# Kernel tuning notes

Measured on AMD Instinct MI355X. Metric: run time of the kernel, lower is better.

## Reference

```python
import jax, jax.numpy as jnp
import numpy as np

NEG_INF = -100000000.0
N, L, E, DIM, V_IN, V_OUT = 64, 512, 128, 512, 32000, 10000
D = 2 * DIM  # encoder output feature dim


def _lstm_layer(x, Wih, Whh, bih, bhh, reverse=False):
    """Single-direction LSTM over (N, L, I) -> (N, L, H). PyTorch gate order i,f,g,o."""
    n = x.shape[0]
    H = Whh.shape[1]
    xg = jnp.einsum('nli,gi->nlg', x, Wih) + bih  # precompute input projections (N, L, 4H)

    def step(carry, g_in):
        h, c = carry
        g = g_in + h @ Whh.T + bhh
        i, f, gg, o = jnp.split(g, 4, axis=-1)
        c = jax.nn.sigmoid(f) * c + jax.nn.sigmoid(i) * jnp.tanh(gg)
        h = jax.nn.sigmoid(o) * jnp.tanh(c)
        return (h, c), h

    init = (jnp.zeros((n, H), x.dtype), jnp.zeros((n, H), x.dtype))
    _, hs = jax.lax.scan(step, init, jnp.swapaxes(xg, 0, 1), reverse=reverse)
    return jnp.swapaxes(hs, 0, 1)


def setup_inputs() -> dict:
    key = jax.random.key(0)
    ks = iter(jax.random.split(key, 40))

    def p(shape):
        return (jax.random.normal(next(ks), shape, jnp.float32) * 0.05)

    inp = {}
    inp['X'] = jax.random.randint(next(ks), (N, L), 0, V_IN)
    sl = jax.random.randint(next(ks), (N,), 1, L + 1)
    inp['seq_len'] = sl.at[0].set(L)  # ensure max length == L as the torch code assumes
    inp['embed_W'] = p((V_IN, E))
    # encoder layer 0 (input E, hidden DIM), fwd + bwd directions
    for tag, I in (('l0f', E), ('l0b', E), ('l1f', D), ('l1b', D)):
        inp[tag + '_Wih'] = p((4 * DIM, I))
        inp[tag + '_Whh'] = p((4 * DIM, DIM))
        inp[tag + '_bih'] = p((4 * DIM,))
        inp[tag + '_bhh'] = p((4 * DIM,))
    for tag in ('Ws', 'Wa', 'Ua'):
        inp[tag + '_W'] = p((D, D))
        inp[tag + '_b'] = p((D,))
    inp['va_W'] = p((1, D))
    inp['va_b'] = p((1,))
    inp['dec_Wih'] = p((4 * D, D))
    inp['dec_Whh'] = p((4 * D, D))
    inp['dec_bih'] = p((4 * D,))
    inp['dec_bhh'] = p((4 * D,))
    inp['cls_W'] = p((V_OUT, D))
    inp['cls_b'] = p((V_OUT,))
    return inp


def reference(X, seq_len, embed_W,
              l0f_Wih, l0f_Whh, l0f_bih, l0f_bhh,
              l0b_Wih, l0b_Whh, l0b_bih, l0b_bhh,
              l1f_Wih, l1f_Whh, l1f_bih, l1f_bhh,
              l1b_Wih, l1b_Whh, l1b_bih, l1b_bhh,
              Ws_W, Ws_b, Wa_W, Wa_b, Ua_W, Ua_b, va_W, va_b,
              dec_Wih, dec_Whh, dec_bih, dec_bhh, cls_W, cls_b):
    emb = embed_W[X]  # (N, L, E)
    h0 = jnp.concatenate([
        _lstm_layer(emb, l0f_Wih, l0f_Whh, l0f_bih, l0f_bhh, reverse=False),
        _lstm_layer(emb, l0b_Wih, l0b_Whh, l0b_bih, l0b_bhh, reverse=True)], axis=-1)
    hid = jnp.concatenate([
        _lstm_layer(h0, l1f_Wih, l1f_Whh, l1f_bih, l1f_bhh, reverse=False),
        _lstm_layer(h0, l1b_Wih, l1b_Whh, l1b_bih, l1b_bhh, reverse=True)], axis=-1)  # (N, L, 2*dim)

    ll = hid.shape[1]
    mask = (jnp.arange(ll)[None, :] >= seq_len[:, None]).astype(hid.dtype)  # 1 where padded
    Ua_h = hid @ Ua_W.T + Ua_b  # hoisted: U_a(hid) is loop-invariant
    s_i = jnp.tanh(hid[:, 0] @ Ws_W.T + Ws_b)  # (N, D)

    outs = []
    for _ in range(11):
        e = (jnp.tanh((s_i @ Wa_W.T + Wa_b)[:, None, :] + Ua_h) @ va_W.T + va_b)[..., 0]  # (N, L)
        att = jax.nn.softmax(e + NEG_INF * mask, axis=-1)
        ci = jnp.einsum('nl,nld->nd', att, hid)  # context (N, D)
        # single-step decoder LSTM; cell state reset to zero each step (as in torch code)
        g = ci @ dec_Wih.T + dec_bih + s_i @ dec_Whh.T + dec_bhh
        i, f, gg, o = jnp.split(g, 4, axis=-1)
        c = jax.nn.sigmoid(i) * jnp.tanh(gg)  # f * 0 == 0
        s_i = jax.nn.sigmoid(o) * jnp.tanh(c)
        outs.append(s_i)

    s = jnp.stack(outs, axis=1)  # (N, 11, D)
    return s @ cls_W.T + cls_b  # (N, 11, num_outclass)
```

## Files before the change

kernel.cpp:

```cpp
#include <hip/hip_runtime.h>
#include <stdint.h>

#define NEG_INF -100000000.0f

typedef unsigned short u16;
typedef unsigned long long u64;
typedef __attribute__((ext_vector_type(8))) short v8s;
typedef __attribute__((ext_vector_type(4))) short v4s;
typedef __attribute__((ext_vector_type(4))) float v4f;

__device__ __forceinline__ float bf2f(u16 h){ return __uint_as_float(((unsigned)h)<<16); }
__device__ __forceinline__ u16 f2bf(float f){
  unsigned u = __float_as_uint(f);
  u = u + 0x7fffu + ((u>>16)&1u);
  return (u16)(u>>16);
}
__device__ __forceinline__ float sigm(float x){ return 1.0f/(1.0f+__expf(-x)); }
__device__ __forceinline__ float ftanh(float x){
  x = fminf(15.0f, fmaxf(-15.0f, x));
  float e = __expf(2.0f*x);
  return (e-1.0f)/(e+1.0f);
}

__device__ __forceinline__ void store_h16(u16* p, u64 a, u64 b){
  __hip_atomic_store((u64*)p,     a, __ATOMIC_RELAXED, __HIP_MEMORY_SCOPE_AGENT);
  __hip_atomic_store((u64*)(p+4), b, __ATOMIC_RELAXED, __HIP_MEMORY_SCOPE_AGENT);
}

struct CvtTab {
  const float* src[31];
  unsigned off[31];
  unsigned n[31];
  unsigned total;
};

__global__ __launch_bounds__(256) void cvt_all(CvtTab tab, u16* __restrict__ arena){
  unsigned e0 = (blockIdx.x*256u + threadIdx.x)*8u;
  if (e0 >= tab.total) return;
  int s = 0;
#pragma unroll 1
  for (int i = 1; i < 31; ++i) if (e0 >= tab.off[i]) s = i;
  unsigned rel = e0 - tab.off[s];
  const float* sp = tab.src[s] + rel;
  unsigned nn = tab.n[s];
  union { u16 h[8]; v8s v; } o;
  if (rel + 8 <= nn) {
    float4 a = *(const float4*)sp;
    float4 b = *(const float4*)(sp+4);
    o.h[0]=f2bf(a.x); o.h[1]=f2bf(a.y); o.h[2]=f2bf(a.z); o.h[3]=f2bf(a.w);
    o.h[4]=f2bf(b.x); o.h[5]=f2bf(b.y); o.h[6]=f2bf(b.z); o.h[7]=f2bf(b.w);
  } else {
#pragma unroll
    for (int k = 0; k < 8; ++k) o.h[k] = (rel + k < nn) ? f2bf(sp[k]) : (u16)0;
  }
  *(v8s*)(arena + e0) = o.v;
}

#define GF_OUTBF16 1
#define GF_TANH    2
#define GF_ACCUM   4

__global__ __launch_bounds__(256) void gemm_bf16(
    const u16* __restrict__ A, long long lda,
    const u16* __restrict__ B,
    const u16* __restrict__ bias1, const u16* __restrict__ bias2,
    void* __restrict__ Cout, long long ldc,
    int M, int Nn, int K, int flags)
{
  __shared__ u16 As[8192];
  __shared__ u16 Bs[8192];
  int tid = threadIdx.x;
  int lane = tid & 63, w = tid >> 6;
  int wm = w >> 1, wn = w & 1;
  int bm = blockIdx.x * 128, bn = blockIdx.y * 128;

  v4f acc[4][4];
#pragma unroll
  for (int i=0;i<4;++i)
#pragma unroll
    for (int j=0;j<4;++j) acc[i][j] = (v4f){0.f,0.f,0.f,0.f};

#pragma unroll 1
  for (int ko = 0; ko < K; ko += 64) {
    __syncthreads();
#pragma unroll
    for (int it = 0; it < 8; ++it) {
      int c = tid + 256*it;
      int half = c >> 10;
      int cc = c & 1023;
      int r = cc >> 3;
      int kcb = cc & 7;
      const u16* src;
      if (half == 0) {
        int row = min(bm + r, M-1);
        src = A + (size_t)row*(size_t)lda + ko + (kcb<<3);
      } else {
        int row = min(bn + r, Nn-1);
        src = B + (size_t)row*(size_t)K + ko + (kcb<<3);
      }
      v8s v = *(const v8s*)src;
      char* base = (char*)(half ? Bs : As);
      *(v8s*)(base + (r<<7) + ((kcb<<4) ^ ((r&7)<<4))) = v;
    }
    __syncthreads();
#pragma unroll
    for (int ks = 0; ks < 2; ++ks) {
      v8s af[4], bfr[4];
#pragma unroll
      for (int mt=0; mt<4; ++mt) {
        int r = wm*64 + mt*16 + (lane & 15);
        int kb = (ks<<6) + ((lane>>4)<<4);
        af[mt] = *(const v8s*)((const char*)As + (r<<7) + (kb ^ ((r&7)<<4)));
      }
#pragma unroll
      for (int nt=0; nt<4; ++nt) {
        int r = wn*64 + nt*16 + (lane & 15);
        int kb = (ks<<6) + ((lane>>4)<<4);
        bfr[nt] = *(const v8s*)((const char*)Bs + (r<<7) + (kb ^ ((r&7)<<4)));
      }
#pragma unroll
      for (int mt=0; mt<4; ++mt)
#pragma unroll
        for (int nt=0; nt<4; ++nt)
          acc[mt][nt] = __builtin_amdgcn_mfma_f32_16x16x32_bf16(af[mt], bfr[nt], acc[mt][nt], 0,0,0);
    }
  }

#pragma unroll
  for (int mt=0; mt<4; ++mt) {
#pragma unroll
    for (int nt=0; nt<4; ++nt) {
      int col = bn + wn*64 + nt*16 + (lane&15);
      if (col >= Nn) continue;
      float b = 0.f;
      if (bias1) b += bf2f(bias1[col]);
      if (bias2) b += bf2f(bias2[col]);
#pragma unroll
      for (int r=0; r<4; ++r) {
        int row = bm + wm*64 + mt*16 + ((lane>>4)<<2) + r;
        if (row >= M) continue;
        float v = acc[mt][nt][r] + b;
        if (flags & GF_ACCUM) v += ((float*)Cout)[(size_t)row*(size_t)ldc + col];
        if (flags & GF_TANH) v = ftanh(v);
        if (flags & GF_OUTBF16) ((u16*)Cout)[(size_t)row*(size_t)ldc + col] = f2bf(v);
        else                    ((float*)Cout)[(size_t)row*(size_t)ldc + col] = v;
      }
    }
  }
}

template<int LAYER>
__global__ __launch_bounds__(256, 1) void lstm_scan(
    const u16* __restrict__ xsrc,
    const int* __restrict__ Xidx,
    const u16* __restrict__ Wih_f, const u16* __restrict__ Wih_b,
    const u16* __restrict__ Whh_f, const u16* __restrict__ Whh_b,
    const u16* __restrict__ bih_f, const u16* __restrict__ bhh_f,
    const u16* __restrict__ bih_b, const u16* __restrict__ bhh_b,
    u16* __restrict__ hbuf,
    unsigned* __restrict__ prog)
{
  constexpr int KX  = (LAYER==0) ? 128 : 1024;
  constexpr int NKC = KX/64;
  __shared__ float glds[8*32*18];
  __shared__ u16   hlds[1024];

  const int tid = threadIdx.x, lane = tid & 63, w = tid >> 6;
  const int kh = w >> 1, gp = w & 1;
  const int dir = blockIdx.x >> 6, bg = (blockIdx.x >> 5) & 1, ug = blockIdx.x & 31;
  const int an = lane & 15, hi = lane >> 4, ak = hi << 3;
  const u16* Wih = dir ? Wih_b : Wih_f;
  const u16* Whh = dir ? Whh_b : Whh_f;
  const int gid = dir*2 + bg;
  unsigned* gprog = prog + gid*32;

  const int g = 2*gp + (an>>3);

  v8s wih_reg[2][NKC];
#pragma unroll
  for (int nt = 0; nt < 2; ++nt) {
    const u16* wp = Wih + ((size_t)g*512 + ug*16 + nt*8 + (an&7))*KX + kh*(KX/2);
#pragma unroll
    for (int kc = 0; kc < NKC; ++kc) {
      wih_reg[nt][kc] = *(const v8s*)(wp + kc*32 + ak);
      asm volatile("" : "+v"(wih_reg[nt][kc]));
    }
  }
  v8s whh_reg[2][8];
#pragma unroll
  for (int nt = 0; nt < 2; ++nt) {
    const u16* wp = Whh + ((size_t)g*512 + ug*16 + nt*8 + (an&7))*512 + kh*256;
#pragma unroll
    for (int kc = 0; kc < 8; ++kc) {
      whh_reg[nt][kc] = *(const v8s*)(wp + kc*32 + ak);
      asm volatile("" : "+v"(whh_reg[nt][kc]));
    }
  }

  const int u_pw = tid & 15, n2 = tid >> 4;
  const int uj_pw = ug*16 + u_pw;
  float bsum[4];
  {
    const u16* bi = dir ? bih_b : bih_f;
    const u16* bh = dir ? bhh_b : bhh_f;
#pragma unroll
    for (int q = 0; q < 4; ++q)
      bsum[q] = bf2f(bi[q*512 + uj_pw]) + bf2f(bh[q*512 + uj_pw]);
  }
  float creg[2] = {0.f, 0.f};

  v8s xreg[2][NKC];
  {
    const int t0 = dir ? 511 : 0;
#pragma unroll
    for (int mt = 0; mt < 2; ++mt) {
      int ng = bg*32 + mt*16 + an;
      const u16* xr;
      if constexpr (LAYER == 0) xr = xsrc + (size_t)Xidx[ng*512 + t0]*128 + kh*64;
      else                      xr = xsrc + ((size_t)(ng*512 + t0) << 10) + kh*512;
#pragma unroll
      for (int kc = 0; kc < NKC; ++kc) xreg[mt][kc] = *(const v8s*)(xr + kc*32 + ak);
    }
  }

  for (int step = 0; step < 512; ++step) {
    const int t     = dir ? (511 - step) : step;
    const int tprev = dir ? (t + 1) : (t - 1);

    v4f acc[2][2];
#pragma unroll
    for (int i=0;i<2;++i){ acc[i][0]=(v4f){0,0,0,0}; acc[i][1]=(v4f){0,0,0,0}; }

    if (step > 0) {
      {
        const u64* pl = (const u64*)gprog;
        int spins = 0;
        for (;;) {
          u64 v = ~0ull;
          if (lane < 16)
            v = __hip_atomic_load(pl + lane, __ATOMIC_RELAXED, __HIP_MEMORY_SCOPE_AGENT);
          bool ok = ((unsigned)v >= (unsigned)step) && ((unsigned)(v>>32) >= (unsigned)step);
          if (__all(ok)) break;
          if (++spins > 4) __builtin_amdgcn_s_sleep(1);
        }
        asm volatile("" ::: "memory");
      }

      v8s haf[2][8];
#pragma unroll
      for (int mt = 0; mt < 2; ++mt) {
        int ng = bg*32 + mt*16 + an;
        const u16* hr = hbuf + ((size_t)(ng*512 + tprev) << 10) + dir*512 + kh*256;
#pragma unroll
        for (int kc = 0; kc < 8; ++kc) haf[mt][kc] = *(const v8s*)(hr + kc*32 + ak);
      }
#pragma unroll
      for (int kc = 0; kc < NKC; ++kc)
#pragma unroll
        for (int nt = 0; nt < 2; ++nt)
#pragma unroll
          for (int mt = 0; mt < 2; ++mt)
            acc[mt][nt] = __builtin_amdgcn_mfma_f32_16x16x32_bf16(xreg[mt][kc], wih_reg[nt][kc], acc[mt][nt], 0,0,0);
#pragma unroll
      for (int kc = 0; kc < 8; ++kc)
#pragma unroll
        for (int nt = 0; nt < 2; ++nt)
#pragma unroll
          for (int mt = 0; mt < 2; ++mt)
            acc[mt][nt] = __builtin_amdgcn_mfma_f32_16x16x32_bf16(haf[mt][kc], whh_reg[nt][kc], acc[mt][nt], 0,0,0);
    } else {
#pragma unroll
      for (int kc = 0; kc < NKC; ++kc)
#pragma unroll
        for (int nt = 0; nt < 2; ++nt)
#pragma unroll
          for (int mt = 0; mt < 2; ++mt)
            acc[mt][nt] = __builtin_amdgcn_mfma_f32_16x16x32_bf16(xreg[mt][kc], wih_reg[nt][kc], acc[mt][nt], 0,0,0);
    }

#pragma unroll
    for (int mt=0; mt<2; ++mt)
#pragma unroll
      for (int nt=0; nt<2; ++nt)
#pragma unroll
        for (int r=0; r<4; ++r) {
          int n = mt*16 + hi*4 + r;
          int u = nt*8 + (an&7);
          glds[((kh*4 + g)*32 + n)*18 + u] = acc[mt][nt][r];
        }
    __syncthreads();

#pragma unroll
    for (int k = 0; k < 2; ++k) {
      int n = k*16 + n2;
      float g0 = glds[(0*32+n)*18+u_pw] + glds[(4*32+n)*18+u_pw] + bsum[0];
      float g1 = glds[(1*32+n)*18+u_pw] + glds[(5*32+n)*18+u_pw] + bsum[1];
      float g2 = glds[(2*32+n)*18+u_pw] + glds[(6*32+n)*18+u_pw] + bsum[2];
      float g3 = glds[(3*32+n)*18+u_pw] + glds[(7*32+n)*18+u_pw] + bsum[3];
      float cn = sigm(g1)*creg[k] + sigm(g0)*ftanh(g2);
      creg[k] = cn;
      hlds[n*16 + u_pw] = f2bf(sigm(g3)*ftanh(cn));
    }

    if (lane < 16) {
      int j = lane >> 1;
      int n = 4*w + (j & 3) + 16*(j >> 2);
      int half = lane & 1;
      u64 a = *(const u64*)&hlds[n*16 + half*8];
      u64 b = *(const u64*)&hlds[n*16 + half*8 + 4];
      store_h16(hbuf + ((size_t)((bg*32+n)*512 + t) << 10) + dir*512 + ug*16 + half*8, a, b);
    }

    if (step < 511) {
      const int tn = dir ? (t - 1) : (t + 1);
#pragma unroll
      for (int mt = 0; mt < 2; ++mt) {
        int ng = bg*32 + mt*16 + an;
        const u16* xr;
        if constexpr (LAYER == 0) xr = xsrc + (size_t)Xidx[ng*512 + tn]*128 + kh*64;
        else                      xr = xsrc + ((size_t)(ng*512 + tn) << 10) + kh*512;
#pragma unroll
        for (int kc = 0; kc < NKC; ++kc) xreg[mt][kc] = *(const v8s*)(xr + kc*32 + ak);
      }
    }

    asm volatile("s_waitcnt vmcnt(0)" ::: "memory");
    __syncthreads();

    if (tid == 0)
      __hip_atomic_store(gprog + ug, (unsigned)(step+1), __ATOMIC_RELAXED, __HIP_MEMORY_SCOPE_AGENT);
  }
}

__global__ __launch_bounds__(256) void attn_step(
    const float* __restrict__ qbuf, const u16* __restrict__ Uah,
    const u16* __restrict__ hid, const int* __restrict__ seq_len,
    const u16* __restrict__ vaW, const u16* __restrict__ vab,
    u16* __restrict__ catb)
{
  int n = blockIdx.x, tid = threadIdx.x;
  __shared__ float qs[1024];
  __shared__ float vas[1024];
  __shared__ float es[512];
  __shared__ float red[8];
  for (int d=tid; d<1024; d+=256){ qs[d]=qbuf[n*1024+d]; vas[d]=bf2f(vaW[d]); }
  __syncthreads();
  int sl = seq_len[n];
  float vb = bf2f(vab[0]);
  for (int l=tid; l<512; l+=256) {
    const u16* up = Uah + ((size_t)n*512 + l)*1024;
    float a = 0.f;
    for (int d=0; d<1024; d+=8) {
      v8s uv = *(const v8s*)(up + d);
#pragma unroll
      for (int e=0;e<8;++e)
        a = fmaf(ftanh(bf2f((u16)uv[e]) + qs[d+e]), vas[d+e], a);
    }
    float ev = a + vb;
    if (l >= sl) ev += NEG_INF;
    es[l] = ev;
  }
  __syncthreads();
  float m = -3.4e38f;
  for (int l=tid; l<512; l+=256) m = fmaxf(m, es[l]);
#pragma unroll
  for (int off=1; off<64; off<<=1) m = fmaxf(m, __shfl_xor(m, off));
  if ((tid&63)==0) red[tid>>6] = m;
  __syncthreads();
  m = fmaxf(fmaxf(red[0],red[1]), fmaxf(red[2],red[3]));
  float s = 0.f;
  for (int l=tid; l<512; l+=256){ float p = __expf(es[l]-m); es[l]=p; s+=p; }
#pragma unroll
  for (int off=1; off<64; off<<=1) s += __shfl_xor(s, off);
  if ((tid&63)==0) red[4+(tid>>6)] = s;
  __syncthreads();
  float inv = 1.f/(red[4]+red[5]+red[6]+red[7]);
  int d0 = tid*4;
  float c0=0,c1=0,c2=0,c3=0;
  for (int l=0; l<512; ++l) {
    float a = es[l];
    const u16* hp = hid + ((size_t)n*512 + l)*1024 + d0;
    v4s hv = *(const v4s*)hp;
    c0 = fmaf(a, bf2f((u16)hv[0]), c0);
    c1 = fmaf(a, bf2f((u16)hv[1]), c1);
    c2 = fmaf(a, bf2f((u16)hv[2]), c2);
    c3 = fmaf(a, bf2f((u16)hv[3]), c3);
  }
  catb[n*2048 + d0 + 0] = f2bf(c0*inv);
  catb[n*2048 + d0 + 1] = f2bf(c1*inv);
  catb[n*2048 + d0 + 2] = f2bf(c2*inv);
  catb[n*2048 + d0 + 3] = f2bf(c3*inv);
}

__global__ void dec_pw(const float* __restrict__ g, u16* __restrict__ scat,
                       u16* __restrict__ catb, int it)
{
  int idx = blockIdx.x*256 + threadIdx.x;
  int n = idx >> 10, d = idx & 1023;
  float gi = g[(size_t)n*4096 + d];
  float gg = g[(size_t)n*4096 + 2048 + d];
  float go = g[(size_t)n*4096 + 3072 + d];
  float c = sigm(gi)*ftanh(gg);
  float s = sigm(go)*ftanh(c);
  u16 hb = f2bf(s);
  scat[((size_t)n*11 + it)*1024 + d] = hb;
  catb[n*2048 + 1024 + d] = hb;
}

__global__ void fill_sentinel(float* out, int nel){
  int i = blockIdx.x*256 + threadIdx.x;
  if (i < nel) out[i] = 12345.0f;
}

extern "C" void kernel_launch(void* const* d_in, const int* in_sizes, int n_in,
                              void* d_out, int out_size, void* d_ws, size_t ws_size,
                              hipStream_t stream)
{
  const int* X      = (const int*)d_in[0];
  const int* seqlen = (const int*)d_in[1];
  float* out = (float*)d_out;
  char* ws = (char*)d_ws;

  struct Seg { int idx; int n; };
  static const Seg segs[31] = {
    {2, 4096000},
    {3, 262144},{4,1048576},{5,2048},{6,2048},
    {7, 262144},{8,1048576},{9,2048},{10,2048},
    {11,2097152},{12,1048576},{13,2048},{14,2048},
    {15,2097152},{16,1048576},{17,2048},{18,2048},
    {19,1048576},{20,1024},
    {21,1048576},{22,1024},
    {23,1048576},{24,1024},
    {25,1024},{26,1},
    {27,4194304},{28,4194304},{29,4096},{30,4096},
    {31,10240000},{32,10000},
  };
  const u16* bp[33];
  CvtTab tab;
  size_t aoff = 0;
  for (int i = 0; i < 31; ++i) {
    bp[segs[i].idx] = (const u16*)(ws) + aoff;
    tab.src[i] = (const float*)d_in[segs[i].idx];
    tab.off[i] = (unsigned)aoff;
    tab.n[i]   = (unsigned)segs[i].n;
    aoff += (size_t)((segs[i].n + 7) & ~7);
  }
  tab.total = (unsigned)aoff;
  size_t arena_bytes = ((aoff*2 + 255) & ~(size_t)255);

  const size_t H0_OFF   = arena_bytes;
  const size_t HID_OFF  = H0_OFF   + 67108864;
  const size_t BAR_OFF  = HID_OFF  + 67108864;
  const size_t CATB_OFF = BAR_OFF  + 16384;
  const size_t QBUF_OFF = CATB_OFF + 262144;
  const size_t GDEC_OFF = QBUF_OFF + 262144;
  const size_t SCAT_OFF = GDEC_OFF + 1048576;
  const size_t NEED     = SCAT_OFF + 1441792;

  if (ws_size < NEED) {
    fill_sentinel<<<(out_size+255)/256, 256, 0, stream>>>(out, out_size);
    return;
  }

  u16*      h0   = (u16*)(ws + H0_OFF);
  u16*      Uah  = (u16*)(ws + H0_OFF);
  u16*      hid  = (u16*)(ws + HID_OFF);
  unsigned* bar  = (unsigned*)(ws + BAR_OFF);
  u16*      catb = (u16*)(ws + CATB_OFF);
  float*    qbuf = (float*)(ws + QBUF_OFF);
  float*    gdec = (float*)(ws + GDEC_OFF);
  u16*      scat = (u16*)(ws + SCAT_OFF);

  hipMemsetAsync(ws + BAR_OFF, 0, 16384, stream);

  {
    unsigned nth = (unsigned)(aoff / 8);
    cvt_all<<<(nth + 255)/256, 256, 0, stream>>>(tab, (u16*)ws);
  }

  lstm_scan<0><<<128, 256, 0, stream>>>(
      bp[2], X, bp[3], bp[7], bp[4], bp[8],
      bp[5], bp[6], bp[9], bp[10], h0, bar);

  lstm_scan<1><<<128, 256, 0, stream>>>(
      h0, nullptr, bp[11], bp[15], bp[12], bp[16],
      bp[13], bp[14], bp[17], bp[18], hid, bar + 1024);

  gemm_bf16<<<dim3(256,8), 256, 0, stream>>>(hid, 1024, bp[23], bp[24], nullptr,
      Uah, 1024, 32768, 1024, 1024, GF_OUTBF16);
  gemm_bf16<<<dim3(1,8), 256, 0, stream>>>(hid, 524288, bp[19], bp[20], nullptr,
      catb + 1024, 2048, 64, 1024, 1024, GF_OUTBF16 | GF_TANH);

  for (int it = 0; it < 11; ++it) {
    gemm_bf16<<<dim3(1,8), 256, 0, stream>>>(catb + 1024, 2048, bp[21], bp[22], nullptr,
        qbuf, 1024, 64, 1024, 1024, 0);
    attn_step<<<64, 256, 0, stream>>>(qbuf, Uah, hid, seqlen, bp[25], bp[26], catb);
    gemm_bf16<<<dim3(1,32), 256, 0, stream>>>(catb, 2048, bp[27], bp[29], bp[30],
        gdec, 4096, 64, 4096, 1024, 0);
    gemm_bf16<<<dim3(1,32), 256, 0, stream>>>(catb + 1024, 2048, bp[28], nullptr, nullptr,
        gdec, 4096, 64, 4096, 1024, GF_ACCUM);
    dec_pw<<<256, 256, 0, stream>>>(gdec, scat, catb, it);
  }

  gemm_bf16<<<dim3(6,79), 256, 0, stream>>>(scat, 1024, bp[31], bp[32], nullptr,
      out, 10000, 704, 10000, 1024, 0);
}
```

Measured before the change: 9.742 ms.

## Split LSTM scan work by hidden units instead of batch groups per block

Each block now owns 8 hidden units for all 64 batch rows (two 32-row chunks processed in sequence) instead of 16 units for 32 rows, so each direction spans 64 unit blocks and the batch split is gone. This halves the weight registers per block. Each block now waits on and updates both progress groups, and layer 1 loads its input activations inline each step instead of prefetching them one step ahead. The change trades register pressure for more serial work per step and more cross-block synchronisation traffic.

```diff
diff --git a/kernel.cpp b/kernel.cpp
--- a/kernel.cpp
+++ b/kernel.cpp
@@ -162,43 +162,43 @@
 {
   constexpr int KX  = (LAYER==0) ? 128 : 1024;
   constexpr int NKC = KX/64;
-  __shared__ float glds[8*32*18];
-  __shared__ u16   hlds[1024];
+  __shared__ float glds[2][8*32*10];
+  __shared__ u16   hlds[2][256];
 
   const int tid = threadIdx.x, lane = tid & 63, w = tid >> 6;
   const int kh = w >> 1, gp = w & 1;
-  const int dir = blockIdx.x >> 6, bg = (blockIdx.x >> 5) & 1, ug = blockIdx.x & 31;
+  const int dir = blockIdx.x >> 6, ug = blockIdx.x & 63;
   const int an = lane & 15, hi = lane >> 4, ak = hi << 3;
   const u16* Wih = dir ? Wih_b : Wih_f;
   const u16* Whh = dir ? Whh_b : Whh_f;
-  const int gid = dir*2 + bg;
-  unsigned* gprog = prog + gid*32;
+  const int gidA = dir*2, gidB = dir*2 + 1;
+  unsigned* progA = prog + gidA*64;
+  unsigned* progB = prog + gidB*64;
 
   const int g = 2*gp + (an>>3);
-
-  v8s wih_reg[2][NKC];
-#pragma unroll
-  for (int nt = 0; nt < 2; ++nt) {
-    const u16* wp = Wih + ((size_t)g*512 + ug*16 + nt*8 + (an&7))*KX + kh*(KX/2);
+  const size_t jrow = (size_t)g*512 + ug*8 + (an&7);
+
+  v8s wih_reg[NKC];
+  {
+    const u16* wp = Wih + jrow*KX + kh*(KX/2);
 #pragma unroll
     for (int kc = 0; kc < NKC; ++kc) {
-      wih_reg[nt][kc] = *(const v8s*)(wp + kc*32 + ak);
-      asm volatile("" : "+v"(wih_reg[nt][kc]));
-    }
-  }
-  v8s whh_reg[2][8];
-#pragma unroll
-  for (int nt = 0; nt < 2; ++nt) {
-    const u16* wp = Whh + ((size_t)g*512 + ug*16 + nt*8 + (an&7))*512 + kh*256;
+      wih_reg[kc] = *(const v8s*)(wp + kc*32 + ak);
+      asm volatile("" : "+v"(wih_reg[kc]));
+    }
+  }
+  v8s whh_reg[8];
+  {
+    const u16* wp = Whh + jrow*512 + kh*256;
 #pragma unroll
     for (int kc = 0; kc < 8; ++kc) {
-      whh_reg[nt][kc] = *(const v8s*)(wp + kc*32 + ak);
-      asm volatile("" : "+v"(whh_reg[nt][kc]));
-    }
-  }
-
-  const int u_pw = tid & 15, n2 = tid >> 4;
-  const int uj_pw = ug*16 + u_pw;
+      whh_reg[kc] = *(const v8s*)(wp + kc*32 + ak);
+      asm volatile("" : "+v"(whh_reg[kc]));
+    }
+  }
+
+  const int u_pw = tid & 7, n2 = tid >> 3;
+  const int uj_pw = ug*8 + u_pw;
   float bsum[4];
   {
     const u16* bi = dir ? bih_b : bih_f;
@@ -209,118 +209,140 @@
   }
   float creg[2] = {0.f, 0.f};
 
-  v8s xreg[2][NKC];
-  {
+  constexpr int XC = (LAYER==0) ? 2 : 1;
+  v8s xreg[2][2][XC];
+  if constexpr (LAYER == 0) {
     const int t0 = dir ? 511 : 0;
 #pragma unroll
-    for (int mt = 0; mt < 2; ++mt) {
-      int ng = bg*32 + mt*16 + an;
-      const u16* xr;
-      if constexpr (LAYER == 0) xr = xsrc + (size_t)Xidx[ng*512 + t0]*128 + kh*64;
-      else                      xr = xsrc + ((size_t)(ng*512 + t0) << 10) + kh*512;
-#pragma unroll
-      for (int kc = 0; kc < NKC; ++kc) xreg[mt][kc] = *(const v8s*)(xr + kc*32 + ak);
-    }
+    for (int c = 0; c < 2; ++c)
+#pragma unroll
+      for (int mt = 0; mt < 2; ++mt) {
+        int ng = c*32 + mt*16 + an;
+        const u16* xr = xsrc + (size_t)Xidx[ng*512 + t0]*128 + kh*64;
+#pragma unroll
+        for (int kc = 0; kc < 2; ++kc) xreg[c][mt][kc] = *(const v8s*)(xr + kc*32 + ak);
+      }
   }
 
   for (int step = 0; step < 512; ++step) {
     const int t     = dir ? (511 - step) : step;
     const int tprev = dir ? (t + 1) : (t - 1);
 
-    v4f acc[2][2];
-#pragma unroll
-    for (int i=0;i<2;++i){ acc[i][0]=(v4f){0,0,0,0}; acc[i][1]=(v4f){0,0,0,0}; }
-
     if (step > 0) {
-      {
-        const u64* pl = (const u64*)gprog;
-        int spins = 0;
-        for (;;) {
-          u64 v = ~0ull;
-          if (lane < 16)
-            v = __hip_atomic_load(pl + lane, __ATOMIC_RELAXED, __HIP_MEMORY_SCOPE_AGENT);
-          bool ok = ((unsigned)v >= (unsigned)step) && ((unsigned)(v>>32) >= (unsigned)step);
-          if (__all(ok)) break;
-          if (++spins > 4) __builtin_amdgcn_s_sleep(1);
+      const u64* pl = (lane < 32) ? ((const u64*)progA + lane)
+                                  : ((const u64*)progB + (lane - 32));
+      int spins = 0;
+      for (;;) {
+        u64 v = __hip_atomic_load(pl, __ATOMIC_RELAXED, __HIP_MEMORY_SCOPE_AGENT);
+        bool ok = ((unsigned)v >= (unsigned)step) && ((unsigned)(v>>32) >= (unsigned)step);
+        if (__all(ok)) break;
+        if (++spins > 4) __builtin_amdgcn_s_sleep(1);
+      }
+      asm volatile("" ::: "memory");
+    }
+
+#pragma unroll
+    for (int c = 0; c < 2; ++c) {
+      v4f acc[2];
+      acc[0] = (v4f){0,0,0,0}; acc[1] = (v4f){0,0,0,0};
+
+      if (step > 0) {
+        v8s haf[2][8];
+#pragma unroll
+        for (int mt = 0; mt < 2; ++mt) {
+          int ng = c*32 + mt*16 + an;
+          const u16* hr = hbuf + ((size_t)(ng*512 + tprev) << 10) + dir*512 + kh*256;
+#pragma unroll
+          for (int kc = 0; kc < 8; ++kc) haf[mt][kc] = *(const v8s*)(hr + kc*32 + ak);
         }
-        asm volatile("" ::: "memory");
-      }
-
-      v8s haf[2][8];
-#pragma unroll
-      for (int mt = 0; mt < 2; ++mt) {
-        int ng = bg*32 + mt*16 + an;
-        const u16* hr = hbuf + ((size_t)(ng*512 + tprev) << 10) + dir*512 + kh*256;
-#pragma unroll
-        for (int kc = 0; kc < 8; ++kc) haf[mt][kc] = *(const v8s*)(hr + kc*32 + ak);
-      }
-#pragma unroll
-      for (int kc = 0; kc < NKC; ++kc)
-#pragma unroll
-        for (int nt = 0; nt < 2; ++nt)
+        if constexpr (LAYER == 0) {
+#pragma unroll
+          for (int kc = 0; kc < 2; ++kc)
+#pragma unroll
+            for (int mt = 0; mt < 2; ++mt)
+              acc[mt] = __builtin_amdgcn_mfma_f32_16x16x32_bf16(xreg[c][mt][kc], wih_reg[kc], acc[mt], 0,0,0);
+        } else {
+          v8s xaf[2][16];
+#pragma unroll
+          for (int mt = 0; mt < 2; ++mt) {
+            int ng = c*32 + mt*16 + an;
+            const u16* xr = xsrc + ((size_t)(ng*512 + t) << 10) + kh*512;
+#pragma unroll
+            for (int kc = 0; kc < 16; ++kc) xaf[mt][kc] = *(const v8s*)(xr + kc*32 + ak);
+          }
+#pragma unroll
+          for (int kc = 0; kc < 16; ++kc)
+#pragma unroll
+            for (int mt = 0; mt < 2; ++mt)
+              acc[mt] = __builtin_amdgcn_mfma_f32_16x16x32_bf16(xaf[mt][kc], wih_reg[kc], acc[mt], 0,0,0);
+        }
+#pragma unroll
+        for (int kc = 0; kc < 8; ++kc)
 #pragma unroll
           for (int mt = 0; mt < 2; ++mt)
-            acc[mt][nt] = __builtin_amdgcn_mfma_f32_16x16x32_bf16(xreg[mt][kc], wih_reg[nt][kc], acc[mt][nt], 0,0,0);
-#pragma unroll
-      for (int kc = 0; kc < 8; ++kc)
-#pragma unroll
-        for (int nt = 0; nt < 2; ++nt)
-#pragma unroll
-          for (int mt = 0; mt < 2; ++mt)
-            acc[mt][nt] = __builtin_amdgcn_mfma_f32_16x16x32_bf16(haf[mt][kc], whh_reg[nt][kc], acc[mt][nt], 0,0,0);
-    } else {
-#pragma unroll
-      for (int kc = 0; kc < NKC; ++kc)
-#pragma unroll
-        for (int nt = 0; nt < 2; ++nt)
-#pragma unroll
-          for (int mt = 0; mt < 2; ++mt)
-            acc[mt][nt] = __builtin_amdgcn_mfma_f32_16x16x32_bf16(xreg[mt][kc], wih_reg[nt][kc], acc[mt][nt], 0,0,0);
-    }
-
-#pragma unroll
-    for (int mt=0; mt<2; ++mt)
-#pragma unroll
-      for (int nt=0; nt<2; ++nt)
+            acc[mt] = __builtin_amdgcn_mfma_f32_16x16x32_bf16(haf[mt][kc], whh_reg[kc], acc[mt], 0,0,0);
+      } else {
+        if constexpr (LAYER == 0) {
+#pragma unroll
+          for (int kc = 0; kc < 2; ++kc)
+#pragma unroll
+            for (int mt = 0; mt < 2; ++mt)
+              acc[mt] = __builtin_amdgcn_mfma_f32_16x16x32_bf16(xreg[c][mt][kc], wih_reg[kc], acc[mt], 0,0,0);
+        } else {
+          v8s xaf[2][16];
+#pragma unroll
+          for (int mt = 0; mt < 2; ++mt) {
+            int ng = c*32 + mt*16 + an;
+            const u16* xr = xsrc + ((size_t)(ng*512 + t) << 10) + kh*512;
+#pragma unroll
+            for (int kc = 0; kc < 16; ++kc) xaf[mt][kc] = *(const v8s*)(xr + kc*32 + ak);
+          }
+#pragma unroll
+          for (int kc = 0; kc < 16; ++kc)
+#pragma unroll
+            for (int mt = 0; mt < 2; ++mt)
+              acc[mt] = __builtin_amdgcn_mfma_f32_16x16x32_bf16(xaf[mt][kc], wih_reg[kc], acc[mt], 0,0,0);
+        }
+      }
+
+#pragma unroll
+      for (int mt=0; mt<2; ++mt)
 #pragma unroll
         for (int r=0; r<4; ++r) {
           int n = mt*16 + hi*4 + r;
-          int u = nt*8 + (an&7);
-          glds[((kh*4 + g)*32 + n)*18 + u] = acc[mt][nt][r];
+          glds[c][((kh*4 + g)*32 + n)*10 + (an&7)] = acc[mt][r];
         }
-    __syncthreads();
-
-#pragma unroll
-    for (int k = 0; k < 2; ++k) {
-      int n = k*16 + n2;
-      float g0 = glds[(0*32+n)*18+u_pw] + glds[(4*32+n)*18+u_pw] + bsum[0];
-      float g1 = glds[(1*32+n)*18+u_pw] + glds[(5*32+n)*18+u_pw] + bsum[1];
-      float g2 = glds[(2*32+n)*18+u_pw] + glds[(6*32+n)*18+u_pw] + bsum[2];
-      float g3 = glds[(3*32+n)*18+u_pw] + glds[(7*32+n)*18+u_pw] + bsum[3];
-      float cn = sigm(g1)*creg[k] + sigm(g0)*ftanh(g2);
-      creg[k] = cn;
-      hlds[n*16 + u_pw] = f2bf(sigm(g3)*ftanh(cn));
-    }
-
-    if (lane < 16) {
-      int j = lane >> 1;
-      int n = 4*w + (j & 3) + 16*(j >> 2);
-      int half = lane & 1;
-      u64 a = *(const u64*)&hlds[n*16 + half*8];
-      u64 b = *(const u64*)&hlds[n*16 + half*8 + 4];
-      store_h16(hbuf + ((size_t)((bg*32+n)*512 + t) << 10) + dir*512 + ug*16 + half*8, a, b);
-    }
-
-    if (step < 511) {
-      const int tn = dir ? (t - 1) : (t + 1);
-#pragma unroll
-      for (int mt = 0; mt < 2; ++mt) {
-        int ng = bg*32 + mt*16 + an;
-        const u16* xr;
-        if constexpr (LAYER == 0) xr = xsrc + (size_t)Xidx[ng*512 + tn]*128 + kh*64;
-        else                      xr = xsrc + ((size_t)(ng*512 + tn) << 10) + kh*512;
-#pragma unroll
-        for (int kc = 0; kc < NKC; ++kc) xreg[mt][kc] = *(const v8s*)(xr + kc*32 + ak);
+      __syncthreads();
+
+      {
+        float g0 = glds[c][(0*32+n2)*10+u_pw] + glds[c][(4*32+n2)*10+u_pw] + bsum[0];
+        float g1 = glds[c][(1*32+n2)*10+u_pw] + glds[c][(5*32+n2)*10+u_pw] + bsum[1];
+        float g2 = glds[c][(2*32+n2)*10+u_pw] + glds[c][(6*32+n2)*10+u_pw] + bsum[2];
+        float g3 = glds[c][(3*32+n2)*10+u_pw] + glds[c][(7*32+n2)*10+u_pw] + bsum[3];
+        float cn = sigm(g1)*creg[c] + sigm(g0)*ftanh(g2);
+        creg[c] = cn;
+        hlds[c][n2*8 + u_pw] = f2bf(sigm(g3)*ftanh(cn));
+      }
+      if (lane < 8) {
+        int nl = w*8 + lane;
+        u64 a = *(const u64*)&hlds[c][nl*8];
+        u64 b = *(const u64*)&hlds[c][nl*8 + 4];
+        store_h16(hbuf + ((size_t)((c*32 + nl)*512 + t) << 10) + dir*512 + ug*8, a, b);
+      }
+    }
+
+    if constexpr (LAYER == 0) {
+      if (step < 511) {
+        const int tn = dir ? (t - 1) : (t + 1);
+#pragma unroll
+        for (int c = 0; c < 2; ++c)
+#pragma unroll
+          for (int mt = 0; mt < 2; ++mt) {
+            int ng = c*32 + mt*16 + an;
+            const u16* xr = xsrc + (size_t)Xidx[ng*512 + tn]*128 + kh*64;
+#pragma unroll
+            for (int kc = 0; kc < 2; ++kc) xreg[c][mt][kc] = *(const v8s*)(xr + kc*32 + ak);
+          }
       }
     }
 
@@ -328,7 +350,9 @@
     __syncthreads();
 
     if (tid == 0)
-      __hip_atomic_store(gprog + ug, (unsigned)(step+1), __ATOMIC_RELAXED, __HIP_MEMORY_SCOPE_AGENT);
+      __hip_atomic_store(progA + ug, (unsigned)(step+1), __ATOMIC_RELAXED, __HIP_MEMORY_SCOPE_AGENT);
+    if (tid == 1)
+      __hip_atomic_store(progB + ug, (unsigned)(step+1), __ATOMIC_RELAXED, __HIP_MEMORY_SCOPE_AGENT);
   }
 }
 
```

Result: slower. 15.73 ms (+61.5%).
